# Performance work log

Measured on AMD Instinct MI355X. Metric: run time of the kernel, lower is better.

Reference implementation:

```python
import jax, jax.numpy as jnp
import numpy as np

B, L, D = 2048, 64, 300   # batch, words per sentence, embedding dim (== kernel_size)
C = 512                    # conv out_channels
H, O = 2048, 1             # fc hidden, fc output


def setup_inputs() -> dict:
    key = jax.random.key(0)
    ks = jax.random.split(key, 8)
    s = 0.05
    return {
        "x1": jax.random.normal(ks[0], (B, L, D), jnp.float32),
        "x2": jax.random.normal(ks[1], (B, L, D), jnp.float32),
        # Conv1d(in=1, out=C, kernel=D) weight is [C,1,D]; stored as [C,D]
        "Wc": jax.random.normal(ks[2], (C, D), jnp.float32) * s,
        "bc": jax.random.normal(ks[3], (C,), jnp.float32) * s,
        "W1": jax.random.normal(ks[4], (H, 2 * C), jnp.float32) * s,
        "b1": jax.random.normal(ks[5], (H,), jnp.float32) * s,
        "W2": jax.random.normal(ks[6], (O, H), jnp.float32) * s,
        "b2": jax.random.normal(ks[7], (O,), jnp.float32) * s,
    }


def reference(x1, x2, Wc, bc, W1, b1, W2, b2):
    # Per-word Conv1d(kernel=D) + ReLU is a full-width filter == linear map D->C.
    # Batch all words in one einsum instead of the original Python loop.
    def encode(x):
        h = jax.nn.relu(jnp.einsum('bld,cd->blc', x, Wc) + bc)  # [B,L,C]
        return jnp.max(h, axis=1)                                # max over words -> [B,C]

    e1 = encode(x1)
    e2 = encode(x2)
    feat = jnp.concatenate([e1 - e2, e1 * e2], axis=1)           # [B,2C]
    h = jnp.tanh(feat @ W1.T + b1)                               # [B,H]
    return h @ W2.T + b2                                         # [B,O]
```

## Files before the change

kernel.cpp:

```cpp
#include <hip/hip_runtime.h>


#define B_SZ 2048
#define L_SZ 64
#define D_SZ 300
#define C_SZ 512
#define H_SZ 2048
#define NKC 40

typedef __bf16 bf16x8 __attribute__((ext_vector_type(8)));
typedef float f32x4 __attribute__((ext_vector_type(4)));

__device__ __forceinline__ unsigned short f2bf(float f) {
  unsigned int u = __float_as_uint(f);
  u += 0x7fffu + ((u >> 16) & 1u);
  return (unsigned short)(u >> 16);
}

__global__ __launch_bounds__(256)
void convert_kernel(const float* __restrict__ Wc, const float* __restrict__ W1,
                    const float* __restrict__ b2,
                    unsigned short* __restrict__ WcSwz, unsigned short* __restrict__ W1Swz,
                    float* __restrict__ out) {
  int id = blockIdx.x * 256 + threadIdx.x;
  if (id < B_SZ) out[id] = b2[0];
  if (id < C_SZ * NKC) {
    int c = id / NKC, kc = id - c * NKC;
    unsigned short tmp[8];
    #pragma unroll
    for (int i = 0; i < 8; ++i) {
      int k = kc * 8 + i;
      tmp[i] = (k < D_SZ) ? f2bf(Wc[c * D_SZ + k]) : (unsigned short)0;
    }
    unsigned short* dst = WcSwz + (((c >> 4) * NKC + kc) * 16 + (c & 15)) * 8;
    *reinterpret_cast<uint4*>(dst) = *reinterpret_cast<uint4*>(tmp);
    return;
  }
  id -= C_SZ * NKC;
  if (id < H_SZ * 128) {
    int j = id >> 7, kc = id & 127;
    const float* src = W1 + (size_t)j * 1024 + kc * 8;
    unsigned short tmp[8];
    #pragma unroll
    for (int i = 0; i < 8; ++i) tmp[i] = f2bf(src[i]);
    unsigned short* dst = W1Swz + (((j >> 4) * 128 + kc) * 16 + (j & 15)) * 8;
    *reinterpret_cast<uint4*>(dst) = *reinterpret_cast<uint4*>(tmp);
  }
}

__global__ __launch_bounds__(512, 2)
void encode_feat_kernel(const float* __restrict__ x1, const float* __restrict__ x2,
                        const unsigned short* __restrict__ WcSwz,
                        const float* __restrict__ bc,
                        unsigned short* __restrict__ featSwz) {
  __shared__ unsigned short xs[2][64 * NKC * 8];
  __shared__ float fs[1024];
  const int tid = threadIdx.x;
  const int wave = tid >> 6, lane = tid & 63;
  const int l16 = lane & 15, quad = lane >> 4;

  for (int i = tid; i < 256; i += 512) {
    int buf = i >> 7, r = i & 127;
    int mt = r >> 5, kc = 38 + ((r >> 4) & 1), l = r & 15;
    *reinterpret_cast<uint4*>(&xs[buf][mt * 5120 + kc * 128 + l * 8]) = make_uint4(0, 0, 0, 0);
  }

  float bias[4];
  #pragma unroll
  for (int nt = 0; nt < 4; ++nt) bias[nt] = bc[wave * 64 + nt * 16 + l16];

  float4 pf0[5], pf1[5];
  auto LOAD = [&](int t) {
    const float* xb = ((t & 1) ? x2 : x1) +
                      (size_t)(blockIdx.x + (t >> 1) * 256) * (L_SZ * D_SZ);
    #pragma unroll
    for (int r = 0; r < 5; ++r) {
      int idx = r * 512 + tid;
      if (idx < 2432) {
        int g = idx >> 4, l = idx & 15;
        int mt = g / 38, c8 = g - mt * 38;
        const float* s = xb + (mt * 16 + l) * D_SZ + c8 * 8;
        pf0[r] = *reinterpret_cast<const float4*>(s);
        pf1[r] = (c8 < 37) ? *reinterpret_cast<const float4*>(s + 4)
                           : make_float4(0.f, 0.f, 0.f, 0.f);
      }
    }
  };
  auto WRITE = [&](int buf) {
    #pragma unroll
    for (int r = 0; r < 5; ++r) {
      int idx = r * 512 + tid;
      if (idx < 2432) {
        int g = idx >> 4, l = idx & 15;
        int mt = g / 38, c8 = g - mt * 38;
        unsigned int w0 = (unsigned int)f2bf(pf0[r].x) | ((unsigned int)f2bf(pf0[r].y) << 16);
        unsigned int w1 = (unsigned int)f2bf(pf0[r].z) | ((unsigned int)f2bf(pf0[r].w) << 16);
        unsigned int w2 = (unsigned int)f2bf(pf1[r].x) | ((unsigned int)f2bf(pf1[r].y) << 16);
        unsigned int w3 = (unsigned int)f2bf(pf1[r].z) | ((unsigned int)f2bf(pf1[r].w) << 16);
        *reinterpret_cast<uint4*>(&xs[buf][mt * 5120 + c8 * 128 + l * 8]) =
            make_uint4(w0, w1, w2, w3);
      }
    }
  };

  LOAD(0);
  WRITE(0);
  __syncthreads();

  const unsigned short* wc_lane = WcSwz + (wave * 4) * 5120 + quad * 128 + l16 * 8;
  float e1[4];
  int cur = 0;

  #pragma unroll 2
  for (int t = 0; t < 16; ++t) {
    if (t < 15) LOAD(t + 1);

    f32x4 acc[4][4];
    #pragma unroll
    for (int mt = 0; mt < 4; ++mt)
      #pragma unroll
      for (int nt = 0; nt < 4; ++nt)
        #pragma unroll
        for (int r = 0; r < 4; ++r) acc[mt][nt][r] = 0.f;

    const unsigned short* xb = &xs[cur][quad * 128 + l16 * 8];
    #pragma unroll
    for (int ks = 0; ks < 10; ++ks) {
      bf16x8 a[4];
      #pragma unroll
      for (int mt = 0; mt < 4; ++mt)
        a[mt] = *reinterpret_cast<const bf16x8*>(xb + mt * 5120 + ks * 512);
      #pragma unroll
      for (int nt = 0; nt < 4; ++nt) {
        bf16x8 bw = *reinterpret_cast<const bf16x8*>(wc_lane + nt * 5120 + ks * 512);
        #pragma unroll
        for (int mt = 0; mt < 4; ++mt)
          acc[mt][nt] = __builtin_amdgcn_mfma_f32_16x16x32_bf16(a[mt], bw, acc[mt][nt], 0, 0, 0);
      }
    }

    #pragma unroll
    for (int nt = 0; nt < 4; ++nt) {
      float v = 0.f;
      #pragma unroll
      for (int mt = 0; mt < 4; ++mt)
        #pragma unroll
        for (int r = 0; r < 4; ++r)
          v = fmaxf(v, acc[mt][nt][r] + bias[nt]);
      v = fmaxf(v, __shfl_xor(v, 16));
      v = fmaxf(v, __shfl_xor(v, 32));
      if (!(t & 1)) {
        e1[nt] = v;
      } else if (quad == 0) {
        int c = wave * 64 + nt * 16 + l16;
        fs[c]       = e1[nt] - v;
        fs[512 + c] = e1[nt] * v;
      }
    }

    __syncthreads();

    if (t & 1) {
      int b = blockIdx.x + (t >> 1) * 256;
      if (tid < 128) {
        unsigned short tmp[8];
        #pragma unroll
        for (int i = 0; i < 8; ++i) tmp[i] = f2bf(fs[tid * 8 + i]);
        *reinterpret_cast<uint4*>(featSwz + (((b >> 4) * 128 + tid) * 16 + (b & 15)) * 8) =
            *reinterpret_cast<uint4*>(tmp);
      }
    }
    if (t < 15) WRITE(cur ^ 1);

    __syncthreads();
    cur ^= 1;
  }
}

__global__ __launch_bounds__(256, 4)
void fc1_kernel(const unsigned short* __restrict__ featSwz,
                const unsigned short* __restrict__ W1Swz,
                const float* __restrict__ b1, const float* __restrict__ W2,
                float* __restrict__ out) {
  const int mbase = blockIdx.x * 32;
  const int tid = threadIdx.x;
  const int wave = tid >> 6, lane = tid & 63;
  const int l16 = lane & 15, quad = lane >> 4;
  const int nbase = blockIdx.y * 128 + wave * 32;

  f32x4 acc[2][2];
  #pragma unroll
  for (int mt = 0; mt < 2; ++mt)
    #pragma unroll
    for (int nt = 0; nt < 2; ++nt)
      #pragma unroll
      for (int r = 0; r < 4; ++r) acc[mt][nt][r] = 0.f;

  #pragma unroll 4
  for (int ks = 0; ks < 32; ++ks) {
    bf16x8 a[2], bw[2];
    #pragma unroll
    for (int mt = 0; mt < 2; ++mt)
      a[mt] = *reinterpret_cast<const bf16x8*>(
          featSwz + (((size_t)(blockIdx.x * 2 + mt) * 128 + ks * 4 + quad) * 16 + l16) * 8);
    #pragma unroll
    for (int nt = 0; nt < 2; ++nt)
      bw[nt] = *reinterpret_cast<const bf16x8*>(
          W1Swz + (((size_t)(blockIdx.y * 8 + wave * 2 + nt) * 128 + ks * 4 + quad) * 16 + l16) * 8);
    #pragma unroll
    for (int mt = 0; mt < 2; ++mt)
      #pragma unroll
      for (int nt = 0; nt < 2; ++nt)
        acc[mt][nt] = __builtin_amdgcn_mfma_f32_16x16x32_bf16(a[mt], bw[nt], acc[mt][nt], 0, 0, 0);
  }

  float c[2][4];
  #pragma unroll
  for (int mt = 0; mt < 2; ++mt)
    #pragma unroll
    for (int r = 0; r < 4; ++r) c[mt][r] = 0.f;

  #pragma unroll
  for (int nt = 0; nt < 2; ++nt) {
    int j = nbase + nt * 16 + l16;
    float bias = b1[j];
    float w2 = W2[j];
    #pragma unroll
    for (int mt = 0; mt < 2; ++mt)
      #pragma unroll
      for (int r = 0; r < 4; ++r) {
        float pre = acc[mt][nt][r] + bias;
        pre = fminf(fmaxf(pre, -15.f), 15.f);
        float ex = __expf(2.f * pre);
        c[mt][r] += w2 * ((ex - 1.f) / (ex + 1.f));
      }
  }
  #pragma unroll
  for (int off = 1; off <= 8; off <<= 1)
    #pragma unroll
    for (int mt = 0; mt < 2; ++mt)
      #pragma unroll
      for (int r = 0; r < 4; ++r)
        c[mt][r] += __shfl_xor(c[mt][r], off);

  if (l16 == 0) {
    #pragma unroll
    for (int mt = 0; mt < 2; ++mt)
      #pragma unroll
      for (int r = 0; r < 4; ++r) {
        int brow = mbase + mt * 16 + quad * 4 + r;
        atomicAdd(&out[brow], c[mt][r]);
      }
  }
}

extern "C" void kernel_launch(void* const* d_in, const int* in_sizes, int n_in,
                              void* d_out, int out_size, void* d_ws, size_t ws_size,
                              hipStream_t stream) {
  const float* x1 = (const float*)d_in[0];
  const float* x2 = (const float*)d_in[1];
  const float* Wc = (const float*)d_in[2];
  const float* bc = (const float*)d_in[3];
  const float* W1 = (const float*)d_in[4];
  const float* b1 = (const float*)d_in[5];
  const float* W2 = (const float*)d_in[6];
  const float* b2 = (const float*)d_in[7];

  char* ws = (char*)d_ws;
  unsigned short* WcSwz   = (unsigned short*)(ws);
  unsigned short* W1Swz   = (unsigned short*)(ws + 327680);
  unsigned short* featSwz = (unsigned short*)(ws + 4521984);

  {
    int total = C_SZ * NKC + H_SZ * 128;
    convert_kernel<<<(total + 255) / 256, 256, 0, stream>>>(Wc, W1, b2, WcSwz, W1Swz,
                                                            (float*)d_out);
  }
  encode_feat_kernel<<<256, 512, 0, stream>>>(x1, x2, WcSwz, bc, featSwz);
  fc1_kernel<<<dim3(B_SZ / 32, H_SZ / 128), 256, 0, stream>>>(featSwz, W1Swz, b1, W2,
                                                              (float*)d_out);
}
```

Before: 563.0 us.

## Warp-specialize encoder: producer waves stream fp32 x into LDS via direct loads

Splits the 8 waves of the encoder block into 4 producer waves and 4 consumer waves. Producers copy the next fp32 x tile straight from global memory into LDS with global_load_lds, skipping the register staging and bf16 conversion. Consumers each compute 128 channels, doubling their accumulator count, and convert fp32 to bf16 as they read A fragments from LDS. The intent is to overlap loads with MFMA and cut staging instructions. The cost is a doubled fp32 LDS footprint (~154KB), which likely drops occupancy to one block per CU, higher register pressure in the consumer waves, and half the waves doing no MFMA work.

```diff
diff --git a/kernel.cpp b/kernel.cpp
--- a/kernel.cpp
+++ b/kernel.cpp
@@ -7,6 +7,8 @@
 #define C_SZ 512
 #define H_SZ 2048
 #define NKC 40
+#define TILE_BYTES 76800
+#define BUFSTRIDE 76928
 
 typedef __bf16 bf16x8 __attribute__((ext_vector_type(8)));
 typedef float f32x4 __attribute__((ext_vector_type(4)));
@@ -15,6 +17,19 @@
   unsigned int u = __float_as_uint(f);
   u += 0x7fffu + ((u >> 16) & 1u);
   return (unsigned short)(u >> 16);
+}
+
+__device__ __forceinline__ bf16x8 cvt8(float4 v0, float4 v1) {
+  bf16x8 r;
+  r[0] = (__bf16)v0.x; r[1] = (__bf16)v0.y; r[2] = (__bf16)v0.z; r[3] = (__bf16)v0.w;
+  r[4] = (__bf16)v1.x; r[5] = (__bf16)v1.y; r[6] = (__bf16)v1.z; r[7] = (__bf16)v1.w;
+  return r;
+}
+
+__device__ __forceinline__ void gload_lds16(const float* g, void* l) {
+  __builtin_amdgcn_global_load_lds(
+      (const __attribute__((address_space(1))) void*)g,
+      (__attribute__((address_space(3))) void*)l, 16, 0, 0);
 }
 
 __global__ __launch_bounds__(256)
@@ -53,127 +68,107 @@
                         const unsigned short* __restrict__ WcSwz,
                         const float* __restrict__ bc,
                         unsigned short* __restrict__ featSwz) {
-  __shared__ unsigned short xs[2][64 * NKC * 8];
-  __shared__ float fs[1024];
+  __shared__ __align__(16) char lds_pool[2 * BUFSTRIDE + 4096];
+  float* fs = reinterpret_cast<float*>(lds_pool + 2 * BUFSTRIDE);
   const int tid = threadIdx.x;
   const int wave = tid >> 6, lane = tid & 63;
   const int l16 = lane & 15, quad = lane >> 4;
 
-  for (int i = tid; i < 256; i += 512) {
-    int buf = i >> 7, r = i & 127;
-    int mt = r >> 5, kc = 38 + ((r >> 4) & 1), l = r & 15;
-    *reinterpret_cast<uint4*>(&xs[buf][mt * 5120 + kc * 128 + l * 8]) = make_uint4(0, 0, 0, 0);
-  }
-
-  float bias[4];
-  #pragma unroll
-  for (int nt = 0; nt < 4; ++nt) bias[nt] = bc[wave * 64 + nt * 16 + l16];
-
-  float4 pf0[5], pf1[5];
-  auto LOAD = [&](int t) {
-    const float* xb = ((t & 1) ? x2 : x1) +
-                      (size_t)(blockIdx.x + (t >> 1) * 256) * (L_SZ * D_SZ);
-    #pragma unroll
-    for (int r = 0; r < 5; ++r) {
-      int idx = r * 512 + tid;
-      if (idx < 2432) {
-        int g = idx >> 4, l = idx & 15;
-        int mt = g / 38, c8 = g - mt * 38;
-        const float* s = xb + (mt * 16 + l) * D_SZ + c8 * 8;
-        pf0[r] = *reinterpret_cast<const float4*>(s);
-        pf1[r] = (c8 < 37) ? *reinterpret_cast<const float4*>(s + 4)
-                           : make_float4(0.f, 0.f, 0.f, 0.f);
+  if (tid < 16) {
+    int bbuf = tid >> 3, o = (tid & 7) * 16;
+    *reinterpret_cast<uint4*>(lds_pool + bbuf * BUFSTRIDE + TILE_BYTES + o) =
+        make_uint4(0, 0, 0, 0);
+  }
+
+  float bias[8], e1[8];
+  if (wave < 4) {
+    #pragma unroll
+    for (int nt = 0; nt < 8; ++nt) bias[nt] = bc[wave * 128 + nt * 16 + l16];
+  } else {
+    const float* xb = x1 + (size_t)blockIdx.x * (L_SZ * D_SZ);
+    for (int j = wave - 4; j < 75; j += 4)
+      gload_lds16(xb + j * 256 + lane * 4, lds_pool + j * 1024);
+    asm volatile("s_waitcnt vmcnt(0)" ::: "memory");
+  }
+  __syncthreads();
+
+  const unsigned short* wcb =
+      WcSwz + (size_t)(wave * 8) * 5120 + quad * 128 + l16 * 8;
+  int buf = 0;
+
+  for (int t = 0; t < 16; ++t) {
+    if (wave >= 4) {
+      if (t < 15) {
+        int tn = t + 1;
+        const float* xb = ((tn & 1) ? x2 : x1) +
+                          (size_t)(blockIdx.x + (tn >> 1) * 256) * (L_SZ * D_SZ);
+        char* dst = lds_pool + (buf ^ 1) * BUFSTRIDE;
+        for (int j = wave - 4; j < 75; j += 4)
+          gload_lds16(xb + j * 256 + lane * 4, dst + j * 1024);
+      }
+      asm volatile("s_waitcnt vmcnt(0)" ::: "memory");
+    } else {
+      const char* xb = lds_pool + buf * BUFSTRIDE;
+      f32x4 acc[4][8];
+      #pragma unroll
+      for (int mt = 0; mt < 4; ++mt)
+        #pragma unroll
+        for (int nt = 0; nt < 8; ++nt)
+          #pragma unroll
+          for (int r = 0; r < 4; ++r) acc[mt][nt][r] = 0.f;
+
+      #pragma unroll
+      for (int ks = 0; ks < 10; ++ks) {
+        bf16x8 a[4];
+        #pragma unroll
+        for (int mt = 0; mt < 4; ++mt) {
+          const char* p = xb + (mt * 16 + l16) * 1200 + ks * 128 + quad * 32;
+          float4 v0 = *reinterpret_cast<const float4*>(p);
+          float4 v1 = *reinterpret_cast<const float4*>(p + 16);
+          a[mt] = cvt8(v0, v1);
+        }
+        #pragma unroll
+        for (int nt = 0; nt < 8; ++nt) {
+          bf16x8 bw = *reinterpret_cast<const bf16x8*>(wcb + nt * 5120 + ks * 512);
+          #pragma unroll
+          for (int mt = 0; mt < 4; ++mt)
+            acc[mt][nt] =
+                __builtin_amdgcn_mfma_f32_16x16x32_bf16(a[mt], bw, acc[mt][nt], 0, 0, 0);
+        }
+      }
+
+      #pragma unroll
+      for (int nt = 0; nt < 8; ++nt) {
+        float v = 0.f;
+        #pragma unroll
+        for (int mt = 0; mt < 4; ++mt)
+          #pragma unroll
+          for (int r = 0; r < 4; ++r)
+            v = fmaxf(v, acc[mt][nt][r] + bias[nt]);
+        v = fmaxf(v, __shfl_xor(v, 16));
+        v = fmaxf(v, __shfl_xor(v, 32));
+        if (!(t & 1)) {
+          e1[nt] = v;
+        } else if (quad == 0) {
+          int c = wave * 128 + nt * 16 + l16;
+          fs[c]       = e1[nt] - v;
+          fs[512 + c] = e1[nt] * v;
+        }
       }
     }
-  };
-  auto WRITE = [&](int buf) {
-    #pragma unroll
-    for (int r = 0; r < 5; ++r) {
-      int idx = r * 512 + tid;
-      if (idx < 2432) {
-        int g = idx >> 4, l = idx & 15;
-        int mt = g / 38, c8 = g - mt * 38;
-        unsigned int w0 = (unsigned int)f2bf(pf0[r].x) | ((unsigned int)f2bf(pf0[r].y) << 16);
-        unsigned int w1 = (unsigned int)f2bf(pf0[r].z) | ((unsigned int)f2bf(pf0[r].w) << 16);
-        unsigned int w2 = (unsigned int)f2bf(pf1[r].x) | ((unsigned int)f2bf(pf1[r].y) << 16);
-        unsigned int w3 = (unsigned int)f2bf(pf1[r].z) | ((unsigned int)f2bf(pf1[r].w) << 16);
-        *reinterpret_cast<uint4*>(&xs[buf][mt * 5120 + c8 * 128 + l * 8]) =
-            make_uint4(w0, w1, w2, w3);
-      }
+
+    __syncthreads();
+
+    if ((t & 1) && tid >= 256 && tid < 384) {
+      int i = tid - 256;
+      int b = blockIdx.x + (t >> 1) * 256;
+      unsigned short tmp[8];
+      #pragma unroll
+      for (int k2 = 0; k2 < 8; ++k2) tmp[k2] = f2bf(fs[i * 8 + k2]);
+      *reinterpret_cast<uint4*>(featSwz + (((b >> 4) * 128 + i) * 16 + (b & 15)) * 8) =
+          *reinterpret_cast<uint4*>(tmp);
     }
-  };
-
-  LOAD(0);
-  WRITE(0);
-  __syncthreads();
-
-  const unsigned short* wc_lane = WcSwz + (wave * 4) * 5120 + quad * 128 + l16 * 8;
-  float e1[4];
-  int cur = 0;
-
-  #pragma unroll 2
-  for (int t = 0; t < 16; ++t) {
-    if (t < 15) LOAD(t + 1);
-
-    f32x4 acc[4][4];
-    #pragma unroll
-    for (int mt = 0; mt < 4; ++mt)
-      #pragma unroll
-      for (int nt = 0; nt < 4; ++nt)
-        #pragma unroll
-        for (int r = 0; r < 4; ++r) acc[mt][nt][r] = 0.f;
-
-    const unsigned short* xb = &xs[cur][quad * 128 + l16 * 8];
-    #pragma unroll
-    for (int ks = 0; ks < 10; ++ks) {
-      bf16x8 a[4];
-      #pragma unroll
-      for (int mt = 0; mt < 4; ++mt)
-        a[mt] = *reinterpret_cast<const bf16x8*>(xb + mt * 5120 + ks * 512);
-      #pragma unroll
-      for (int nt = 0; nt < 4; ++nt) {
-        bf16x8 bw = *reinterpret_cast<const bf16x8*>(wc_lane + nt * 5120 + ks * 512);
-        #pragma unroll
-        for (int mt = 0; mt < 4; ++mt)
-          acc[mt][nt] = __builtin_amdgcn_mfma_f32_16x16x32_bf16(a[mt], bw, acc[mt][nt], 0, 0, 0);
-      }
-    }
-
-    #pragma unroll
-    for (int nt = 0; nt < 4; ++nt) {
-      float v = 0.f;
-      #pragma unroll
-      for (int mt = 0; mt < 4; ++mt)
-        #pragma unroll
-        for (int r = 0; r < 4; ++r)
-          v = fmaxf(v, acc[mt][nt][r] + bias[nt]);
-      v = fmaxf(v, __shfl_xor(v, 16));
-      v = fmaxf(v, __shfl_xor(v, 32));
-      if (!(t & 1)) {
-        e1[nt] = v;
-      } else if (quad == 0) {
-        int c = wave * 64 + nt * 16 + l16;
-        fs[c]       = e1[nt] - v;
-        fs[512 + c] = e1[nt] * v;
-      }
-    }
-
-    __syncthreads();
-
-    if (t & 1) {
-      int b = blockIdx.x + (t >> 1) * 256;
-      if (tid < 128) {
-        unsigned short tmp[8];
-        #pragma unroll
-        for (int i = 0; i < 8; ++i) tmp[i] = f2bf(fs[tid * 8 + i]);
-        *reinterpret_cast<uint4*>(featSwz + (((b >> 4) * 128 + tid) * 16 + (b & 15)) * 8) =
-            *reinterpret_cast<uint4*>(tmp);
-      }
-    }
-    if (t < 15) WRITE(cur ^ 1);
-
-    __syncthreads();
-    cur ^= 1;
+    buf ^= 1;
   }
 }
 
```

Measured after the change: 884.0 us. 57.0% more time.
